# Performance work log

Measured on AMD Instinct MI355X. Metric: run time of the kernel, lower is better.

Reference implementation:

```python
import jax, jax.numpy as jnp
import numpy as np

# Hard-coded 36-node detector graph from the source (1-indexed), 220 directed edges.
E_SRC = [1,2,3,4,5,6,7,8,9,10,11,12,13,14,15,16,17,18,19,20,21,22,23,24,25,26,27,28,29,30,31,32,33,34,35,36,4,3,8,7,19,20,15,16,35,36,31,32,11,12,11,11,11,12,12,12,6,5,25,26,28,25,9,9,9,10,10,10,1,2,3,4,5,6,7,8,9,10,11,12,13,14,15,16,17,18,17,18,19,20,16,15,31,32,36,35,3,4,7,8,6,5,25,28,14,9,12,11,1,4,2,3,4,1,6,7,8,5,10,11,12,9,14,15,16,13,18,19,20,17,22,23,24,21,26,27,28,25,30,31,32,29,34,35,36,33,33,34,1,2,14,13,30,29,23,22,21,24,22,21,36,33,4,31,30,15,27,28,18,17,10,9,14,19,18,5,8,1,19,20,21,22,23,24,25,26,27,28,29,30,31,32,33,34,35,36,25,26,13,14,30,29,24,21,23,22,33,34,1,2,28,27,10,9,12,15,22,21,11,10]
E_DST = [2,3,4,1,6,7,8,5,10,11,12,9,14,15,16,13,18,19,20,17,22,23,24,21,26,27,28,25,30,31,32,29,34,35,36,33,33,34,1,2,14,13,30,29,23,22,21,24,22,21,36,33,4,31,30,15,27,28,18,17,10,9,14,19,18,5,8,1,19,20,21,22,23,24,25,26,27,28,29,30,31,32,33,34,35,36,25,26,13,14,30,29,24,21,23,22,33,34,1,2,28,27,10,9,12,15,22,21,11,10,1,2,3,4,5,6,7,8,9,10,11,12,13,14,15,16,17,18,19,20,21,22,23,24,25,26,27,28,29,30,31,32,33,34,35,36,4,3,8,7,19,20,15,16,35,36,31,32,11,12,11,11,11,12,12,12,6,5,25,26,28,25,9,9,9,10,10,10,1,2,3,4,5,6,7,8,9,10,11,12,13,14,15,16,17,18,17,18,19,20,16,15,31,32,36,35,3,4,7,8,6,5,25,28,14,9,12,11,1,4]

B = 20000   # graphs per batch
P = 36      # nodes per graph
N = B * P


def setup_inputs() -> dict:
    key = jax.random.key(0)
    ks = jax.random.split(key, 12)
    src = np.asarray(E_SRC, np.int32) - 1
    dst = np.asarray(E_DST, np.int32) - 1
    offs = (np.arange(B, dtype=np.int32) * P)[:, None]
    edge_index = jnp.asarray(np.stack([(src[None, :] + offs).reshape(-1),
                                       (dst[None, :] + offs).reshape(-1)]))  # [2, B*220]
    batch_index = jnp.asarray(np.repeat(np.arange(B, dtype=np.int32), P))  # [N]
    x = jax.random.normal(ks[0], (N, 2), jnp.float32)
    pos = jax.random.normal(ks[1], (N, 3), jnp.float32)  # unused by forward (faithful to source)

    def lin_w(k, fi, fo):
        s = 1.0 / np.sqrt(fi)
        return jax.random.uniform(k, (fi, fo), jnp.float32, -s, s)

    def lin_b(k, fo):
        return jax.random.uniform(k, (fo,), jnp.float32, -0.05, 0.05)

    return {
        "x": x, "edge_index": edge_index, "pos": pos, "batch_index": batch_index,
        "W0": lin_w(ks[2], 2, 4),   "b0": lin_b(ks[3], 4),
        "W1": lin_w(ks[4], 4, 12),  "b1": lin_b(ks[5], 12),
        "W2": lin_w(ks[6], 12, 16), "b2": lin_b(ks[7], 16),
        "W3": lin_w(ks[8], 16, 32), "b3": lin_b(ks[9], 32),
        "Wfc": lin_w(ks[10], 64, 7), "bfc": lin_b(ks[11], 7),
    }


def reference(x, edge_index, pos, batch_index, W0, b0, W1, b1, W2, b2, W3, b3, Wfc, bfc):
    del pos  # present in the torch signature but unused
    src, dst = edge_index[0], edge_index[1]
    n = x.shape[0]
    # GCN symmetric normalization with self-loops: deg = 1 + in-degree
    deg = jax.ops.segment_sum(jnp.ones(src.shape, x.dtype), dst, num_segments=n) + 1.0
    inv = deg ** -0.5
    enorm = inv[src] * inv[dst]   # edge norm
    snorm = inv * inv             # self-loop norm (deg^-1)

    def gcn_conv(h, W, b):
        h = h @ W  # [n, fo]
        agg = jax.ops.segment_sum(h[src] * enorm[:, None], dst, num_segments=n)
        return agg + h * snorm[:, None] + b

    h = jax.nn.relu(gcn_conv(x, W0, b0))
    h = jax.nn.relu(gcn_conv(h, W1, b1))
    # dropout(0.2) is identity in eval mode
    h = jax.nn.relu(gcn_conv(h, W2, b2))
    h = jax.nn.relu(gcn_conv(h, W3, b3))

    gmp = jax.ops.segment_max(h, batch_index, num_segments=B)
    counts = jax.ops.segment_sum(jnp.ones((n,), h.dtype), batch_index, num_segments=B)
    gap = jax.ops.segment_sum(h, batch_index, num_segments=B) / counts[:, None]
    hidden = jnp.concatenate([gmp, gap], axis=1)  # [B, 64]
    out = jax.nn.relu(hidden @ Wfc + bfc)         # [B, 7]
    return (out, hidden)
```

## Files before the change

kernel.cpp:

```cpp
#include <hip/hip_runtime.h>

typedef __attribute__((ext_vector_type(2))) float f32x2;
typedef __attribute__((ext_vector_type(4))) float f32x4;

#define NGRAPH 20000
#define GPB 7
#define STRIDE 36
#define SB (STRIDE * 4)
#define BOFF 64
#define HSTR 68
#define HID_OFF (252 * STRIDE)
#define WFC_OFF (HID_OFF + GPB * HSTR)

static __constant__ int c_indeg[36] = {
    7,5,5,7,6,5,5,6,9,9,9,9,5,7,7,5,5,6,6,5,7,7,5,5,7,5,5,7,5,6,6,5,6,5,5,6
};
static __constant__ signed char c_adj[36][9] = {
    {3,7,9,6,1,18,10,0,0},      {0,6,7,2,19,0,0,0,0},
    {1,3,33,32,20,0,0,0,0},     {2,10,0,32,21,33,9,0,0},
    {7,9,5,27,22,26,0,0,0},     {4,6,26,23,27,0,0,0,0},
    {5,7,1,24,0,0,0,0,0},       {6,9,4,0,25,1,0,0,0},
    {11,24,27,9,13,18,17,26,14},{8,27,24,3,10,4,7,0,27},
    {9,0,11,21,35,32,3,28,20},  {10,13,8,20,30,29,14,29,21},
    {15,19,18,13,30,0,0,0,0},   {12,18,8,19,14,31,11,0,0},
    {13,11,8,15,29,32,28,0,0},  {14,12,28,33,29,0,0,0,0},
    {19,25,17,34,24,0,0,0,0},   {16,24,8,18,35,25,0,0,0},
    {17,8,0,19,13,12,0,0,0},    {18,1,16,12,13,0,0,0,0},
    {23,30,11,2,31,10,21,0,0},  {20,35,10,3,34,11,22,0,0},
    {21,34,4,35,23,0,0,0,0},    {22,31,5,30,20,0,0,0,0},
    {27,6,16,25,17,8,9,0,0},    {24,7,17,26,16,0,0,0,0},
    {25,5,8,27,4,0,0,0,0},      {26,4,9,5,24,9,8,0,0},
    {31,15,10,14,29,0,0,0,0},   {28,14,11,11,15,30,0,0,0},
    {29,11,12,31,20,23,0,0,0},  {30,13,28,23,20,0,0,0,0},
    {35,3,10,14,2,33,0,0,0},    {32,2,15,3,34,0,0,0,0},
    {33,16,35,22,21,0,0,0,0},   {34,10,17,32,21,22,0,0,0},
};
static __constant__ float c_inv[36] = {
    0.35355339f,0.40824829f,0.40824829f,0.35355339f,0.37796447f,0.40824829f,
    0.40824829f,0.37796447f,0.31622777f,0.31622777f,0.31622777f,0.31622777f,
    0.40824829f,0.35355339f,0.35355339f,0.40824829f,0.40824829f,0.37796447f,
    0.37796447f,0.40824829f,0.35355339f,0.35355339f,0.40824829f,0.40824829f,
    0.35355339f,0.40824829f,0.40824829f,0.35355339f,0.40824829f,0.37796447f,
    0.37796447f,0.40824829f,0.37796447f,0.40824829f,0.40824829f,0.37796447f,
};

static __device__ __forceinline__ f32x2 relu2(f32x2 v) {
    return __builtin_elementwise_max(v, (f32x2){0.f, 0.f});
}

extern "C" __global__ __launch_bounds__(256, 4)
void gcn_fused(const float* __restrict__ x,
               const float* __restrict__ W0, const float* __restrict__ b0,
               const float* __restrict__ W1, const float* __restrict__ b1,
               const float* __restrict__ W2, const float* __restrict__ b2,
               const float* __restrict__ W3, const float* __restrict__ b3,
               const float* __restrict__ Wfc, const float* __restrict__ bfc,
               float* __restrict__ out)
{
    __shared__ float L[252 * STRIDE + GPB * HSTR + 448];

    const int t = threadIdx.x;
    float* wfc_s = &L[WFC_OFF];
    for (int i = t; i < 448; i += 256) wfc_s[i] = Wfc[i];

    const int g = t / 36;
    const int v = t - g * 36;
    const bool act = (g < GPB);
    const int gq = act ? g : GPB - 1;
    const int vc = act ? v : 0;
    const int G  = blockIdx.x * GPB + g;
    const int Gc = (act && G < NGRAPH) ? G : 0;

    const int nd = c_indeg[vc];
    const float inv_v = c_inv[vc];
    int aoff[9];
#pragma unroll
    for (int k = 0; k < 9; ++k)
        aoff[k] = (gq * 36 + (int)c_adj[vc][k]) * SB;
    float* srow = &L[(gq * 36 + vc) * STRIDE];
    const char* Lb = (const char*)L;

    f32x2 h0a, h0b;
    {
        const float2 xv = ((const float2*)x)[(size_t)Gc * 36 + vc];
        const float s0 = xv.x * inv_v, s1 = xv.y * inv_v;
        if (act) { srow[0] = s0; srow[1] = s1; }
        __syncthreads();
        f32x2 c = {s0, s1};
#pragma unroll
        for (int k = 0; k < 5; ++k) c += *(const f32x2*)(Lb + aoff[k]);
        if (nd > 5) c += *(const f32x2*)(Lb + aoff[5]);
        if (nd > 6) c += *(const f32x2*)(Lb + aoff[6]);
        if (nd > 7) { c += *(const f32x2*)(Lb + aoff[7]);
                      c += *(const f32x2*)(Lb + aoff[8]); }
        const float a0 = c.x * inv_v, a1 = c.y * inv_v;
        const f32x2 a0v = {a0, a0}, a1v = {a1, a1};
        const f32x2* W0v = (const f32x2*)W0;
        const f32x2* b0v = (const f32x2*)b0;
        h0a = relu2(__builtin_elementwise_fma(a0v, W0v[0],
                    __builtin_elementwise_fma(a1v, W0v[2], b0v[0])));
        h0b = relu2(__builtin_elementwise_fma(a0v, W0v[1],
                    __builtin_elementwise_fma(a1v, W0v[3], b0v[1])));
    }

    f32x2 h1[6];
    {
        const f32x2 iv = {inv_v, inv_v};
        const f32x2 s0 = h0a * iv, s1 = h0b * iv;
        if (act) *(f32x4*)&srow[16] = (f32x4){s0.x, s0.y, s1.x, s1.y};
        __syncthreads();
        f32x4 c = {s0.x, s0.y, s1.x, s1.y};
#pragma unroll
        for (int k = 0; k < 5; ++k) c += *(const f32x4*)(Lb + aoff[k] + BOFF);
        if (nd > 5) c += *(const f32x4*)(Lb + aoff[5] + BOFF);
        if (nd > 6) c += *(const f32x4*)(Lb + aoff[6] + BOFF);
        if (nd > 7) { c += *(const f32x4*)(Lb + aoff[7] + BOFF);
                      c += *(const f32x4*)(Lb + aoff[8] + BOFF); }
        float a[4];
#pragma unroll
        for (int i = 0; i < 4; ++i) a[i] = c[i] * inv_v;
        f32x2 z[6];
        const f32x2* b1v = (const f32x2*)b1;
#pragma unroll
        for (int j = 0; j < 6; ++j) z[j] = b1v[j];
        const f32x2* W1v = (const f32x2*)W1;
#pragma unroll
        for (int i = 0; i < 4; ++i) {
            const f32x2 av = {a[i], a[i]};
#pragma unroll
            for (int j = 0; j < 6; ++j)
                z[j] = __builtin_elementwise_fma(av, W1v[i * 6 + j], z[j]);
        }
#pragma unroll
        for (int j = 0; j < 6; ++j) h1[j] = relu2(z[j]);
    }

    f32x2 h2[8];
    {
        const f32x2 iv = {inv_v, inv_v};
        f32x2 s[6];
#pragma unroll
        for (int j = 0; j < 6; ++j) s[j] = h1[j] * iv;
        if (act) {
            *(f32x4*)&srow[0] = (f32x4){s[0].x, s[0].y, s[1].x, s[1].y};
            *(f32x4*)&srow[4] = (f32x4){s[2].x, s[2].y, s[3].x, s[3].y};
            *(f32x4*)&srow[8] = (f32x4){s[4].x, s[4].y, s[5].x, s[5].y};
        }
        __syncthreads();
        f32x4 c0 = {s[0].x, s[0].y, s[1].x, s[1].y};
        f32x4 c1 = {s[2].x, s[2].y, s[3].x, s[3].y};
        f32x4 c2 = {s[4].x, s[4].y, s[5].x, s[5].y};
#pragma unroll
        for (int k = 0; k < 5; ++k) {
            const char* base = Lb + aoff[k];
            c0 += *(const f32x4*)(base);
            c1 += *(const f32x4*)(base + 16);
            c2 += *(const f32x4*)(base + 32);
        }
        if (nd > 5) { const char* base = Lb + aoff[5];
            c0 += *(const f32x4*)(base); c1 += *(const f32x4*)(base + 16);
            c2 += *(const f32x4*)(base + 32); }
        if (nd > 6) { const char* base = Lb + aoff[6];
            c0 += *(const f32x4*)(base); c1 += *(const f32x4*)(base + 16);
            c2 += *(const f32x4*)(base + 32); }
        if (nd > 7) {
            const char* ba = Lb + aoff[7];
            c0 += *(const f32x4*)(ba); c1 += *(const f32x4*)(ba + 16);
            c2 += *(const f32x4*)(ba + 32);
            const char* bb = Lb + aoff[8];
            c0 += *(const f32x4*)(bb); c1 += *(const f32x4*)(bb + 16);
            c2 += *(const f32x4*)(bb + 32);
        }
        float a[12];
#pragma unroll
        for (int i = 0; i < 4; ++i) {
            a[i] = c0[i] * inv_v; a[4 + i] = c1[i] * inv_v; a[8 + i] = c2[i] * inv_v;
        }
        f32x2 z[8];
        const f32x2* b2v = (const f32x2*)b2;
#pragma unroll
        for (int j = 0; j < 8; ++j) z[j] = b2v[j];
        const f32x2* W2v = (const f32x2*)W2;
#pragma unroll
        for (int i = 0; i < 12; ++i) {
            const f32x2 av = {a[i], a[i]};
#pragma unroll
            for (int j = 0; j < 8; ++j)
                z[j] = __builtin_elementwise_fma(av, W2v[i * 8 + j], z[j]);
        }
#pragma unroll
        for (int j = 0; j < 8; ++j) h2[j] = relu2(z[j]);
    }

    f32x2 h3[16];
    {
        const f32x2 iv = {inv_v, inv_v};
        f32x2 s[8];
#pragma unroll
        for (int j = 0; j < 8; ++j) s[j] = h2[j] * iv;
        if (act) {
#pragma unroll
            for (int q = 0; q < 4; ++q)
                *(f32x4*)&srow[16 + q * 4] =
                    (f32x4){s[2*q].x, s[2*q].y, s[2*q+1].x, s[2*q+1].y};
        }
        __syncthreads();
        f32x4 c0 = {s[0].x, s[0].y, s[1].x, s[1].y};
        f32x4 c1 = {s[2].x, s[2].y, s[3].x, s[3].y};
        f32x4 c2 = {s[4].x, s[4].y, s[5].x, s[5].y};
        f32x4 c3 = {s[6].x, s[6].y, s[7].x, s[7].y};
#pragma unroll
        for (int k = 0; k < 5; ++k) {
            const char* base = Lb + aoff[k] + BOFF;
            c0 += *(const f32x4*)(base);      c1 += *(const f32x4*)(base + 16);
            c2 += *(const f32x4*)(base + 32); c3 += *(const f32x4*)(base + 48);
        }
        if (nd > 5) { const char* base = Lb + aoff[5] + BOFF;
            c0 += *(const f32x4*)(base);      c1 += *(const f32x4*)(base + 16);
            c2 += *(const f32x4*)(base + 32); c3 += *(const f32x4*)(base + 48); }
        if (nd > 6) { const char* base = Lb + aoff[6] + BOFF;
            c0 += *(const f32x4*)(base);      c1 += *(const f32x4*)(base + 16);
            c2 += *(const f32x4*)(base + 32); c3 += *(const f32x4*)(base + 48); }
        if (nd > 7) {
            const char* ba = Lb + aoff[7] + BOFF;
            c0 += *(const f32x4*)(ba);      c1 += *(const f32x4*)(ba + 16);
            c2 += *(const f32x4*)(ba + 32); c3 += *(const f32x4*)(ba + 48);
            const char* bb = Lb + aoff[8] + BOFF;
            c0 += *(const f32x4*)(bb);      c1 += *(const f32x4*)(bb + 16);
            c2 += *(const f32x4*)(bb + 32); c3 += *(const f32x4*)(bb + 48);
        }
        float a[16];
#pragma unroll
        for (int i = 0; i < 4; ++i) {
            a[i] = c0[i] * inv_v;      a[4 + i] = c1[i] * inv_v;
            a[8 + i] = c2[i] * inv_v;  a[12 + i] = c3[i] * inv_v;
        }
        f32x2 z[16];
        const f32x2* b3v = (const f32x2*)b3;
#pragma unroll
        for (int j = 0; j < 16; ++j) z[j] = b3v[j];
        const f32x2* W3v = (const f32x2*)W3;
#pragma unroll
        for (int i = 0; i < 16; ++i) {
            const f32x2 av = {a[i], a[i]};
#pragma unroll
            for (int j = 0; j < 16; ++j)
                z[j] = __builtin_elementwise_fma(av, W3v[i * 16 + j], z[j]);
        }
#pragma unroll
        for (int j = 0; j < 16; ++j) h3[j] = relu2(z[j]);
    }

    if (act) {
#pragma unroll
        for (int q = 0; q < 4; ++q)
            *(f32x4*)&srow[q * 4] =
                (f32x4){h3[2*q].x, h3[2*q].y, h3[2*q+1].x, h3[2*q+1].y};
    }
    __syncthreads();
    if (act) {
#pragma unroll
        for (int q = 0; q < 4; ++q)
            *(f32x4*)&srow[16 + q * 4] =
                (f32x4){h3[8+2*q].x, h3[8+2*q].y, h3[9+2*q].x, h3[9+2*q].y};
    }
    __syncthreads();

    float* hid = &L[HID_OFF];
    if (t < GPB * 32) {
        const int pg = t >> 5, pf = t & 31;
        const float* col = &L[(pg * 36) * STRIDE + pf];
        float mx = -1e30f, sm = 0.f;
#pragma unroll
        for (int u = 0; u < 36; ++u) {
            const float val = col[u * STRIDE];
            mx = fmaxf(mx, val); sm += val;
        }
        const float gap = sm * (1.0f / 36.0f);
        hid[pg * HSTR + pf] = mx;
        hid[pg * HSTR + 32 + pf] = gap;
        const int PG = blockIdx.x * GPB + pg;
        if (PG < NGRAPH) {
            float* ho = out + (size_t)NGRAPH * 7 + (size_t)PG * 64;
            ho[pf] = mx; ho[32 + pf] = gap;
        }
    }
    __syncthreads();

    if (t < GPB * 7) {
        const int fg = t / 7, o = t - fg * 7;
        float acc = bfc[o];
        const float* hh = &hid[fg * HSTR];
#pragma unroll
        for (int j = 0; j < 64; ++j)
            acc = fmaf(hh[j], wfc_s[j * 7 + o], acc);
        const int FG = blockIdx.x * GPB + fg;
        if (FG < NGRAPH) out[(size_t)FG * 7 + o] = fmaxf(acc, 0.f);
    }
}

extern "C" void kernel_launch(void* const* d_in, const int* in_sizes, int n_in,
                              void* d_out, int out_size, void* d_ws, size_t ws_size,
                              hipStream_t stream) {
    (void)in_sizes; (void)n_in; (void)d_ws; (void)ws_size; (void)out_size;
    const float* x   = (const float*)d_in[0];
    const float* W0  = (const float*)d_in[4];
    const float* b0  = (const float*)d_in[5];
    const float* W1  = (const float*)d_in[6];
    const float* b1  = (const float*)d_in[7];
    const float* W2  = (const float*)d_in[8];
    const float* b2  = (const float*)d_in[9];
    const float* W3  = (const float*)d_in[10];
    const float* b3  = (const float*)d_in[11];
    const float* Wfc = (const float*)d_in[12];
    const float* bfc = (const float*)d_in[13];
    float* out = (float*)d_out;

    const int nblocks = (NGRAPH + GPB - 1) / GPB;
    hipLaunchKernelGGL(gcn_fused, dim3(nblocks), dim3(256), 0, stream,
                       x, W0, b0, W1, b1, W2, b2, W3, b3, Wfc, bfc, out);
}
```

Before: 34.66 us.

## Shrink graphs per block, drop LDS FC staging, compute FC via warp shuffles

Reduces graphs per block from 7 to 6 and raises the launch-bounds occupancy hint from 4 to 5 blocks per CU. The LDS buffers for the hidden vector and the Wfc copy are removed. The final FC layer is now computed with a shuffle-based reduction across 32 lanes, with weights read straight from global memory, which drops one __syncthreads. The aim is to cut LDS use so more blocks fit per CU, at the cost of more blocks overall, tighter register limits, and idle threads in each block.

```diff
diff --git a/kernel.cpp b/kernel.cpp
--- a/kernel.cpp
+++ b/kernel.cpp
@@ -4,13 +4,10 @@
 typedef __attribute__((ext_vector_type(4))) float f32x4;
 
 #define NGRAPH 20000
-#define GPB 7
+#define GPB 6
 #define STRIDE 36
 #define SB (STRIDE * 4)
 #define BOFF 64
-#define HSTR 68
-#define HID_OFF (252 * STRIDE)
-#define WFC_OFF (HID_OFF + GPB * HSTR)
 
 static __constant__ int c_indeg[36] = {
     7,5,5,7,6,5,5,6,9,9,9,9,5,7,7,5,5,6,6,5,7,7,5,5,7,5,5,7,5,6,6,5,6,5,5,6
@@ -48,7 +45,7 @@
     return __builtin_elementwise_max(v, (f32x2){0.f, 0.f});
 }
 
-extern "C" __global__ __launch_bounds__(256, 4)
+extern "C" __global__ __launch_bounds__(256, 5)
 void gcn_fused(const float* __restrict__ x,
                const float* __restrict__ W0, const float* __restrict__ b0,
                const float* __restrict__ W1, const float* __restrict__ b1,
@@ -57,12 +54,9 @@
                const float* __restrict__ Wfc, const float* __restrict__ bfc,
                float* __restrict__ out)
 {
-    __shared__ float L[252 * STRIDE + GPB * HSTR + 448];
+    __shared__ float L[GPB * 36 * STRIDE];
 
     const int t = threadIdx.x;
-    float* wfc_s = &L[WFC_OFF];
-    for (int i = t; i < 448; i += 256) wfc_s[i] = Wfc[i];
-
     const int g = t / 36;
     const int v = t - g * 36;
     const bool act = (g < GPB);
@@ -266,9 +260,9 @@
     }
     __syncthreads();
 
-    float* hid = &L[HID_OFF];
     if (t < GPB * 32) {
         const int pg = t >> 5, pf = t & 31;
+        const int PG = blockIdx.x * GPB + pg;
         const float* col = &L[(pg * 36) * STRIDE + pf];
         float mx = -1e30f, sm = 0.f;
 #pragma unroll
@@ -277,25 +271,32 @@
             mx = fmaxf(mx, val); sm += val;
         }
         const float gap = sm * (1.0f / 36.0f);
-        hid[pg * HSTR + pf] = mx;
-        hid[pg * HSTR + 32 + pf] = gap;
-        const int PG = blockIdx.x * GPB + pg;
         if (PG < NGRAPH) {
             float* ho = out + (size_t)NGRAPH * 7 + (size_t)PG * 64;
             ho[pf] = mx; ho[32 + pf] = gap;
         }
-    }
-    __syncthreads();
-
-    if (t < GPB * 7) {
-        const int fg = t / 7, o = t - fg * 7;
-        float acc = bfc[o];
-        const float* hh = &hid[fg * HSTR];
-#pragma unroll
-        for (int j = 0; j < 64; ++j)
-            acc = fmaf(hh[j], wfc_s[j * 7 + o], acc);
-        const int FG = blockIdx.x * GPB + fg;
-        if (FG < NGRAPH) out[(size_t)FG * 7 + o] = fmaxf(acc, 0.f);
+        float p[7];
+        const float* wr0 = Wfc + pf * 7;
+        const float* wr1 = Wfc + (32 + pf) * 7;
+#pragma unroll
+        for (int o = 0; o < 7; ++o)
+            p[o] = fmaf(mx, wr0[o], gap * wr1[o]);
+#pragma unroll
+        for (int m = 16; m >= 1; m >>= 1) {
+#pragma unroll
+            for (int o = 0; o < 7; ++o)
+                p[o] += __shfl_xor(p[o], m, 32);
+        }
+        if (pf < 7 && PG < NGRAPH) {
+            float w = p[0];
+            w = (pf == 1) ? p[1] : w;
+            w = (pf == 2) ? p[2] : w;
+            w = (pf == 3) ? p[3] : w;
+            w = (pf == 4) ? p[4] : w;
+            w = (pf == 5) ? p[5] : w;
+            w = (pf == 6) ? p[6] : w;
+            out[(size_t)PG * 7 + pf] = fmaxf(w + bfc[pf], 0.f);
+        }
     }
 }
 
```

New measurement: 35.77 us. 3.2% more time.
